# Kernel tuning notes

Hardware: AMD Instinct MI355X
Metric: run time of the kernel (lower is better)

The kernel has to match this reference:

```python
import jax, jax.numpy as jnp
import numpy as np

B, L, D_MODEL = 2, 2048, 256
D_STATE, D_CONV, EXPAND, HEADDIM = 128, 4, 4, 64
D_INNER = EXPAND * D_MODEL            # 1024
NHEADS = D_INNER // HEADDIM           # 16
CONV_DIM = D_INNER + 2 * D_STATE      # 1280
D_IN_PROJ = 2 * D_INNER + 2 * D_STATE + NHEADS  # 2320
CHUNK = 256
GN_EPS = float(np.finfo(np.float32).eps)
RMS_EPS = 1e-5


def _silu(x):
    return x * jax.nn.sigmoid(x)


def _segsum(x):
    # x: (..., T) -> (..., T, T); out[i, j] = sum_{j<k<=i} x[k] for i>=j else -inf
    T = x.shape[-1]
    cs = jnp.cumsum(x, -1)
    d = cs[..., :, None] - cs[..., None, :]
    mask = jnp.tril(jnp.ones((T, T), bool))
    return jnp.where(mask, d, -jnp.inf)


def _ssd(X, A, Bm, Cm):
    # Chunked SSD (Mamba2 ssd_minimal_discrete). X:(b,l,h,p) already dt-scaled,
    # A:(b,l,h) = dt * (-exp(A_log)), Bm/Cm:(b,l,n) with ngroups=1.
    b, l, h, p = X.shape
    c = l // CHUNK
    Xc = X.reshape(b, c, CHUNK, h, p)
    Ac = jnp.transpose(A.reshape(b, c, CHUNK, h), (0, 3, 1, 2))  # (b,h,c,Q)
    Bc = Bm.reshape(b, c, CHUNK, -1)
    Cc = Cm.reshape(b, c, CHUNK, -1)
    A_cs = jnp.cumsum(Ac, -1)                                    # (b,h,c,Q)
    Lmat = jnp.exp(_segsum(Ac))                                  # (b,h,c,Q,Q)
    CB = jnp.einsum('bcln,bcsn->bcls', Cc, Bc)                   # (b,c,Q,Q)
    Y_diag = jnp.einsum('bhcls,bcshp->bclhp', Lmat * CB[:, None], Xc)
    decay_states = jnp.exp(A_cs[..., -1:] - A_cs)                # (b,h,c,Q)
    states = jnp.einsum('bcln,bhcl,bclhp->bchpn', Bc, decay_states, Xc)
    states = jnp.concatenate([jnp.zeros_like(states[:, :1]), states], 1)  # (b,c+1,h,p,n)
    decay_chunk = jnp.exp(_segsum(jnp.pad(A_cs[..., -1], ((0, 0), (0, 0), (1, 0)))))  # (b,h,c+1,c+1)
    new_states = jnp.einsum('bhzc,bchpn->bzhpn', decay_chunk, states)[:, :-1]
    state_decay = jnp.exp(A_cs)                                  # (b,h,c,Q)
    Y_off = jnp.einsum('bcln,bchpn,bhcl->bclhp', Cc, new_states, state_decay)
    return (Y_diag + Y_off).reshape(b, l, h, p)


def _mamba2(u, in_w, conv_w, conv_b, dt_bias, A_log, Dh, norm_w, out_w):
    # u: (b, l, d_model)
    b, l, _ = u.shape
    zxbcdt = u @ in_w.T                                          # (b,l,D_IN_PROJ)
    z = zxbcdt[..., :D_INNER]
    xBC = zxbcdt[..., D_INNER:D_INNER + CONV_DIM]
    dt = jax.nn.softplus(zxbcdt[..., -NHEADS:] + dt_bias)        # (b,l,h)
    # causal depthwise conv over time
    xc = jnp.transpose(xBC, (0, 2, 1))                           # (b,C,l)
    xc = jax.lax.conv_general_dilated(xc, conv_w, (1,), [(D_CONV - 1, 0)],
                                      dimension_numbers=('NCH', 'OIH', 'NCH'),
                                      feature_group_count=CONV_DIM)
    xBC = _silu(jnp.transpose(xc + conv_b[None, :, None], (0, 2, 1)))
    x = xBC[..., :D_INNER].reshape(b, l, NHEADS, HEADDIM)
    Bm = xBC[..., D_INNER:D_INNER + D_STATE]
    Cm = xBC[..., D_INNER + D_STATE:]
    A = dt * (-jnp.exp(A_log))                                   # (b,l,h)
    y = _ssd(dt[..., None] * x, A, Bm, Cm) + x * Dh[None, None, :, None]
    y = y.reshape(b, l, D_INNER) * _silu(z)                      # gated
    y = y * jax.lax.rsqrt(jnp.mean(y * y, -1, keepdims=True) + RMS_EPS) * norm_w
    return y @ out_w.T                                           # (b,l,d_model)


def _resmamba(x, gn_w, gn_b, fp, bp, proj_w, proj_b):
    # GroupNorm(1, C) over (C, L) per sample
    mu = jnp.mean(x, (1, 2), keepdims=True)
    var = jnp.mean((x - mu) ** 2, (1, 2), keepdims=True)
    xn = (x - mu) * jax.lax.rsqrt(var + GN_EPS) * gn_w[None, :, None] + gn_b[None, :, None]
    t = jnp.transpose(xn, (0, 2, 1))                             # (B,L,C)
    fwd = _mamba2(t, *fp)
    bwd = jnp.flip(_mamba2(jnp.flip(t, 1), *bp), 1)
    r = jnp.concatenate([fwd + t, bwd + t], -1)                  # (B,L,2C)
    pr = r @ proj_w.T + proj_b                                   # (B,L,C)
    return x + jnp.transpose(pr, (0, 2, 1))


def setup_inputs():
    key = jax.random.key(0)
    ks = jax.random.split(key, 4)
    s = 0.02
    inp = {
        'x': jax.random.normal(ks[0], (B, D_MODEL, L), jnp.float32),
        'gn_w': jnp.ones((D_MODEL,), jnp.float32),
        'gn_b': jnp.zeros((D_MODEL,), jnp.float32),
        'proj_w': s * jax.random.normal(ks[1], (D_MODEL, 2 * D_MODEL), jnp.float32),
        'proj_b': jnp.zeros((D_MODEL,), jnp.float32),
    }
    for i, p in enumerate(('f', 'b')):
        kk = jax.random.split(ks[2 + i], 5)
        inp[p + '_in_w'] = s * jax.random.normal(kk[0], (D_IN_PROJ, D_MODEL), jnp.float32)
        inp[p + '_conv_w'] = s * jax.random.normal(kk[1], (CONV_DIM, 1, D_CONV), jnp.float32)
        inp[p + '_conv_b'] = jnp.zeros((CONV_DIM,), jnp.float32)
        inp[p + '_dt_bias'] = 0.1 * jax.random.normal(kk[2], (NHEADS,), jnp.float32)
        inp[p + '_A_log'] = jnp.log(jax.random.uniform(kk[3], (NHEADS,), jnp.float32, 1.0, 16.0))
        inp[p + '_D'] = jnp.ones((NHEADS,), jnp.float32)
        inp[p + '_norm_w'] = jnp.ones((D_INNER,), jnp.float32)
        inp[p + '_out_w'] = s * jax.random.normal(kk[4], (D_MODEL, D_INNER), jnp.float32)
    return inp


def reference(x, gn_w, gn_b, proj_w, proj_b,
              f_in_w, f_conv_w, f_conv_b, f_dt_bias, f_A_log, f_D, f_norm_w, f_out_w,
              b_in_w, b_conv_w, b_conv_b, b_dt_bias, b_A_log, b_D, b_norm_w, b_out_w):
    fp = (f_in_w, f_conv_w, f_conv_b, f_dt_bias, f_A_log, f_D, f_norm_w, f_out_w)
    bp = (b_in_w, b_conv_w, b_conv_b, b_dt_bias, b_A_log, b_D, b_norm_w, b_out_w)
    return _resmamba(x, gn_w, gn_b, fp, bp, proj_w, proj_b)
```

## Files before the change

kernel.cpp:

```cpp
#include <hip/hip_runtime.h>
#include <hip/hip_bf16.h>
#include <math.h>

using bf16 = __hip_bfloat16;

#define L_SEQ   2048
#define DMODEL  256
#define DINNER  1024
#define DSTATE  128
#define NH      16
#define HD      64
#define CONVDIM 1280
#define DPROJ   2320
#define NCHK    8
#define CT      256
#define BATCH   2
#define M_TOT   (BATCH*L_SEQ)

#define ACS_N   (BATCH*NH*NCHK*CT)
#define ST_N    ((size_t)BATCH*NCHK*NH*HD*DSTATE)
#define CB_N    ((size_t)BATCH*NCHK*CT*CT)

typedef __bf16 bf16x8_t __attribute__((ext_vector_type(8)));
typedef __bf16 bf16x4_t __attribute__((ext_vector_type(4)));
typedef float  f32x4_t  __attribute__((ext_vector_type(4)));

__device__ __forceinline__ float tof(bf16 v){ return __bfloat162float(v); }
__device__ __forceinline__ bf16  tob(float v){ return __float2bfloat16(v); }
__device__ __forceinline__ float expdec(float a){ return __expf(fminf(a, 0.f)); }

__global__ __launch_bounds__(256) void k_front(
    const float* __restrict__ iw0, const float* __restrict__ iw1, const float* __restrict__ pw,
    bf16* __restrict__ inw_bf, bf16* __restrict__ projw_bf,
    const float* __restrict__ ow0, const float* __restrict__ ow1,
    bf16* __restrict__ owt, bf16* __restrict__ psum,
    const float* __restrict__ x, float2* __restrict__ pbuf){
  __shared__ __bf16 tile[64][65];
  __shared__ float sh[8];
  int bz = blockIdx.x, t = threadIdx.x;
  if (bz < 1160){
    int dir = bz >= 580; int sub = dir ? bz - 580 : bz;
    const float* src = dir ? iw1 : iw0;
    bf16* dst = inw_bf + (size_t)dir*DPROJ*DMODEL;
    int i = (sub*256 + t)*4;
    float4 v = *(const float4*)(src + i);
    dst[i]   = tob(v.x); dst[i+1] = tob(v.y);
    dst[i+2] = tob(v.z); dst[i+3] = tob(v.w);
  } else if (bz < 1288){
    int i = ((bz-1160)*256 + t)*4;
    float4 v = *(const float4*)(pw + i);
    projw_bf[i]   = tob(v.x); projw_bf[i+1] = tob(v.y);
    projw_bf[i+2] = tob(v.z); projw_bf[i+3] = tob(v.w);
  } else if (bz < 1416){
    int sub = bz - 1288;
    int dir = sub >> 6; int tid = sub & 63;
    int k0 = (tid >> 2)*64, j0 = (tid & 3)*64;
    const float* src = dir ? ow1 : ow0;
    bf16* dst = owt + (size_t)dir*DINNER*DMODEL;
    #pragma unroll
    for (int it = 0; it < 2; ++it){
      int idx = t + it*256; int jj = idx >> 3; int k8 = (idx & 7)*8;
      float4 va = *(const float4*)&src[(size_t)(j0+jj)*DINNER + k0 + k8];
      float4 vb = *(const float4*)&src[(size_t)(j0+jj)*DINNER + k0 + k8 + 4];
      tile[k8+0][jj] = (__bf16)va.x; tile[k8+1][jj] = (__bf16)va.y;
      tile[k8+2][jj] = (__bf16)va.z; tile[k8+3][jj] = (__bf16)va.w;
      tile[k8+4][jj] = (__bf16)vb.x; tile[k8+5][jj] = (__bf16)vb.y;
      tile[k8+6][jj] = (__bf16)vb.z; tile[k8+7][jj] = (__bf16)vb.w;
    }
    __syncthreads();
    #pragma unroll
    for (int it = 0; it < 2; ++it){
      int idx = t + it*256; int kr = idx >> 3; int j8 = (idx & 7)*8;
      bf16x8_t o;
      #pragma unroll
      for (int i = 0; i < 8; ++i) o[i] = tile[kr][j8+i];
      *(bf16x8_t*)&dst[(size_t)(k0+kr)*DMODEL + j0 + j8] = o;
    }
  } else if (bz < 1448){
    int i = ((bz - 1416)*256 + t)*8;
    int j = i & 255;
    const float* row = pw + (size_t)(i >> 8)*(2*DMODEL);
    bf16x8_t o;
    #pragma unroll
    for (int c = 0; c < 8; ++c) o[c] = (__bf16)(row[j+c] + row[256+j+c]);
    *(bf16x8_t*)&psum[i] = o;
  } else {
    int sub = bz - 1448;
    int blk = sub & 127, b = sub >> 7;
    const float4* p = (const float4*)(x + (size_t)b*(DMODEL*L_SEQ) + (size_t)blk*4096);
    float s = 0.f, ss = 0.f;
    #pragma unroll
    for (int k = 0; k < 4; ++k){
      float4 v = p[t + k*256];
      s  += v.x + v.y + v.z + v.w;
      ss += v.x*v.x + v.y*v.y + v.z*v.z + v.w*v.w;
    }
    for (int o = 32; o > 0; o >>= 1){ s += __shfl_down(s, o, 64); ss += __shfl_down(ss, o, 64); }
    if ((t & 63) == 0){ sh[(t>>6)*2] = s; sh[(t>>6)*2+1] = ss; }
    __syncthreads();
    if (t == 0){
      s  = sh[0]+sh[2]+sh[4]+sh[6];
      ss = sh[1]+sh[3]+sh[5]+sh[7];
      pbuf[b*128 + blk] = make_float2(s, ss);
    }
  }
}

__global__ __launch_bounds__(256) void k_wt(const bf16* __restrict__ P, const bf16* __restrict__ owt,
                                            bf16* __restrict__ W,
                                            const float* __restrict__ x, const float* __restrict__ gw,
                                            const float* __restrict__ gb, const float2* __restrict__ pbuf,
                                            bf16* __restrict__ t_out){
  __shared__ __align__(16) bf16 lds[2][(128+64)*40];
  __shared__ float tile[64][65];
  __shared__ float sh[4];
  int bz6 = blockIdx.x;
  int t = threadIdx.x;
  if (bz6 < 64){
    int dir = bz6 & 1;
    int m0 = (bz6 >> 5)*128, n0 = ((bz6 >> 1) & 15)*64;
    int wave = t >> 6, lane = t & 63;
    int wm = (wave & 1)*64, wn = (wave >> 1)*32;
    int lrow = lane & 15, quad = lane >> 4, lk8 = quad*8;

    int r0 = t >> 2, o0 = (t & 3)*8;
    int r1 = r0 + 64;
    const bf16* Ap0 = P + (size_t)(m0 + r0)*(2*DMODEL) + dir*DMODEL + o0;
    const bf16* Ap1 = P + (size_t)(m0 + r1)*(2*DMODEL) + dir*DMODEL + o0;
    const bf16* Bp  = owt + (size_t)dir*DINNER*DMODEL + (size_t)(n0 + r0)*DMODEL + o0;

    f32x4_t acc[4][2];
    #pragma unroll
    for (int i = 0; i < 4; ++i){ acc[i][0] = (f32x4_t){0,0,0,0}; acc[i][1] = (f32x4_t){0,0,0,0}; }

    int nit = DMODEL >> 5;
    uint4 a0 = *(const uint4*)Ap0;
    uint4 a1 = *(const uint4*)Ap1;
    uint4 b0 = *(const uint4*)Bp;
    int st = 0;
    *(uint4*)&lds[0][r0*40 + o0] = a0;
    *(uint4*)&lds[0][r1*40 + o0] = a1;
    *(uint4*)&lds[0][(128 + r0)*40 + o0] = b0;
    __syncthreads();
    for (int it = 0; it < nit; ++it){
      bool more = (it+1 < nit);
      if (more){
        int kk = (it+1) << 5;
        a0 = *(const uint4*)(Ap0 + kk);
        a1 = *(const uint4*)(Ap1 + kk);
        b0 = *(const uint4*)(Bp + kk);
      }
      const bf16* cs = lds[st];
      bf16x8_t af[4], bfr[2];
      #pragma unroll
      for (int mi = 0; mi < 4; ++mi) af[mi] = *(const bf16x8_t*)&cs[(wm + mi*16 + lrow)*40 + lk8];
      #pragma unroll
      for (int ni = 0; ni < 2; ++ni) bfr[ni] = *(const bf16x8_t*)&cs[(128 + wn + ni*16 + lrow)*40 + lk8];
      #pragma unroll
      for (int mi = 0; mi < 4; ++mi)
        #pragma unroll
        for (int ni = 0; ni < 2; ++ni)
          acc[mi][ni] = __builtin_amdgcn_mfma_f32_16x16x32_bf16(af[mi], bfr[ni], acc[mi][ni], 0, 0, 0);
      if (more){
        st ^= 1;
        *(uint4*)&lds[st][r0*40 + o0] = a0;
        *(uint4*)&lds[st][r1*40 + o0] = a1;
        *(uint4*)&lds[st][(128 + r0)*40 + o0] = b0;
        __syncthreads();
      }
    }
    bf16* Wd = W + (size_t)dir*DMODEL*DINNER;
    #pragma unroll
    for (int mi = 0; mi < 4; ++mi)
      #pragma unroll
      for (int ni = 0; ni < 2; ++ni)
        #pragma unroll
        for (int r = 0; r < 4; ++r){
          int m = m0 + wm + mi*16 + quad*4 + r;
          int n = n0 + wn + ni*16 + lrow;
          Wd[(size_t)m*DINNER + n] = tob(acc[mi][ni][r]);
        }
  } else {
    int sub = bz6 - 64;
    int l0 = (sub & 31)*64, c0 = ((sub >> 5) & 3)*64, b = sub >> 7;
    int tid = t;
    float s = 0.f, ss = 0.f;
    if (tid < 128){ float2 v = pbuf[b*128 + tid]; s = v.x; ss = v.y; }
    for (int o = 32; o > 0; o >>= 1){ s += __shfl_down(s, o, 64); ss += __shfl_down(ss, o, 64); }
    if (tid < 128 && (tid & 63) == 0){ sh[(tid>>6)*2] = s; sh[(tid>>6)*2+1] = ss; }
    __syncthreads();
    float inv = 1.f/(float)(DMODEL*L_SEQ);
    float s0 = sh[0]+sh[2], ss0 = sh[1]+sh[3];
    float mu = s0*inv, var = ss0*inv - mu*mu;
    float istd = rsqrtf(fmaxf(var, 0.f) + 1.1920929e-07f);

    int lx = tid & 63, cy = tid >> 6;
    for (int cc = cy; cc < 64; cc += 4){
      float v = x[(size_t)b*DMODEL*L_SEQ + (size_t)(c0+cc)*L_SEQ + l0+lx];
      tile[cc][lx] = (v - mu)*istd;
    }
    __syncthreads();
    int cx = tid & 63, ly = tid >> 6;
    float w = gw[c0+cx], bb = gb[c0+cx];
    for (int ll = ly; ll < 64; ll += 4)
      t_out[((size_t)(b*L_SEQ) + l0+ll)*DMODEL + c0+cx] = tob(tile[cx][ll]*w + bb);
  }
}

__global__ __launch_bounds__(512) void gemm_inproj(const bf16* __restrict__ A, const bf16* __restrict__ B,
                                                   bf16* __restrict__ z, bf16* __restrict__ xbc,
                                                   float* __restrict__ dtb,
                                                   const float* __restrict__ db0, const float* __restrict__ db1){
  __shared__ __align__(16) bf16 lds[2][(128+128)*40];
  const int lda = DMODEL, ldb = DMODEL, N = DPROJ;
  int dir = blockIdx.z;
  const bf16* Bd = B + (size_t)dir*(size_t)N*ldb;
  int orig = blockIdx.x;
  int swz = (orig & 7)*76 + (orig >> 3);
  int m0 = (swz & 31)*128;
  int n0 = (swz >> 5)*128;
  int t = threadIdx.x;
  int wave = t >> 6, lane = t & 63;
  int wm = (wave & 1)*64, wn = (wave >> 1)*32;
  int lrow = lane & 15, quad = lane >> 4, lk8 = quad*8;

  int rA = t >> 2, oA = (t & 3)*8;
  int amA = m0 + rA;
  if (dir) amA = (amA & ~(L_SEQ-1)) | ((L_SEQ-1) - (amA & (L_SEQ-1)));
  int bnA = n0 + rA; if (bnA > N-1) bnA = N-1;
  const bf16* Ap = A + (size_t)amA*lda + oA;
  const bf16* Bp = Bd + (size_t)bnA*ldb + oA;

  f32x4_t acc[4][2];
  #pragma unroll
  for (int i = 0; i < 4; ++i){ acc[i][0] = (f32x4_t){0,0,0,0}; acc[i][1] = (f32x4_t){0,0,0,0}; }

  int nit = 8;
  uint4 a0 = *(const uint4*)Ap;
  uint4 b0 = *(const uint4*)Bp;
  int st = 0;
  *(uint4*)&lds[0][rA*40 + oA] = a0;
  *(uint4*)&lds[0][(128 + rA)*40 + oA] = b0;
  __syncthreads();
  for (int it = 0; it < nit; ++it){
    bool more = (it+1 < nit);
    if (more){
      int kk = (it+1) << 5;
      a0 = *(const uint4*)(Ap + kk);
      b0 = *(const uint4*)(Bp + kk);
    }
    const bf16* cs = lds[st];
    bf16x8_t bfr[2];
    #pragma unroll
    for (int ni = 0; ni < 2; ++ni) bfr[ni] = *(const bf16x8_t*)&cs[(128 + wn + ni*16 + lrow)*40 + lk8];
    #pragma unroll
    for (int mi = 0; mi < 4; ++mi){
      bf16x8_t af = *(const bf16x8_t*)&cs[(wm + mi*16 + lrow)*40 + lk8];
      #pragma unroll
      for (int ni = 0; ni < 2; ++ni)
        acc[mi][ni] = __builtin_amdgcn_mfma_f32_16x16x32_bf16(af, bfr[ni], acc[mi][ni], 0, 0, 0);
    }
    if (more){
      st ^= 1;
      *(uint4*)&lds[st][rA*40 + oA] = a0;
      *(uint4*)&lds[st][(128 + rA)*40 + oA] = b0;
      __syncthreads();
    }
  }

  if (n0 < DINNER + CONVDIM){
    __syncthreads();
    __bf16* outs = (__bf16*)lds;
    #pragma unroll
    for (int mi = 0; mi < 4; ++mi)
      #pragma unroll
      for (int ni = 0; ni < 2; ++ni)
        #pragma unroll
        for (int r = 0; r < 4; ++r)
          outs[(wm + mi*16 + quad*4 + r)*132 + wn + ni*16 + lrow] = (__bf16)acc[mi][ni][r];
    __syncthreads();
    bf16* dst; int ldd, c0;
    if (n0 < DINNER){ dst = z   + (size_t)dir*M_TOT*DINNER;  ldd = DINNER;  c0 = n0; }
    else            { dst = xbc + (size_t)dir*M_TOT*CONVDIM; ldd = CONVDIM; c0 = n0 - DINNER; }
    #pragma unroll
    for (int itv = 0; itv < 4; ++itv){
      int v = t + itv*512;
      int row = v >> 4, cb = v & 15;
      *(bf16x8_t*)&dst[(size_t)(m0+row)*ldd + c0 + cb*8] =
          *(const bf16x8_t*)&outs[row*132 + cb*8];
    }
  } else {
    const float* db = dir ? db1 : db0;
    float* dtp = dtb + (size_t)dir*((size_t)M_TOT*NH);
    #pragma unroll
    for (int mi = 0; mi < 4; ++mi)
      #pragma unroll
      for (int ni = 0; ni < 2; ++ni)
        #pragma unroll
        for (int r = 0; r < 4; ++r){
          int m = m0 + wm + mi*16 + quad*4 + r;
          int n = n0 + wn + ni*16 + lrow;
          if (n < N){
            int h = n - (DINNER + CONVDIM);
            float xx = acc[mi][ni][r] + db[h];
            dtp[(size_t)m*NH + h] = (xx > 20.f) ? xx : log1pf(expf(xx));
          }
        }
  }
}

__global__ __launch_bounds__(256) void gemm_final(const bf16* __restrict__ y, const bf16* __restrict__ tb,
                                                  const bf16* __restrict__ W, const bf16* __restrict__ psum,
                                                  const float* __restrict__ x, const float* __restrict__ pb,
                                                  float* __restrict__ out){
  __shared__ __align__(16) bf16 lds[2][(32+64)*72];
  __shared__ float tile[32][65];
  int orig = blockIdx.x;
  int swz = (orig & 7)*64 + (orig >> 3);
  int mt_ = swz & 127, nt_ = swz >> 7;
  int m0 = mt_*32, n0 = nt_*64;
  int t = threadIdx.x;
  int wave = t >> 6, lane = t & 63;
  int lrow = lane & 15, quad = lane >> 4, lk8 = quad*8;
  int wn = wave*16;

  f32x4_t acc[2];
  acc[0] = (f32x4_t){0,0,0,0}; acc[1] = (f32x4_t){0,0,0,0};

  int rowA = t >> 3, oA = (t & 7)*8;
  int rowB0 = t >> 3, oB0 = (t & 7)*8;
  int rowB1 = (t + 256) >> 3, oB1 = (t & 7)*8;

  #pragma unroll
  for (int ph = 0; ph < 3; ++ph){
    const bf16 *Ab, *Bb; int lda, ldb, K, rev;
    if (ph == 0){ Ab = y;                             lda = DINNER; K = DINNER; Bb = W;                             ldb = DINNER; rev = 0; }
    else if (ph == 1){ Ab = y + (size_t)M_TOT*DINNER; lda = DINNER; K = DINNER; Bb = W + (size_t)DMODEL*DINNER;     ldb = DINNER; rev = 1; }
    else { Ab = tb; lda = DMODEL; K = DMODEL; Bb = psum; ldb = DMODEL; rev = 0; }

    int am = m0 + rowA;
    if (rev) am = (am & ~(L_SEQ-1)) | ((L_SEQ-1) - (am & (L_SEQ-1)));
    const bf16* Ap  = Ab + (size_t)am*lda + oA;
    const bf16* Bp0 = Bb + (size_t)(n0 + rowB0)*ldb + oB0;
    const bf16* Bp1 = Bb + (size_t)(n0 + rowB1)*ldb + oB1;

    int nit = K >> 6;
    uint4 au  = *(const uint4*)Ap;
    uint4 bu0 = *(const uint4*)Bp0;
    uint4 bu1 = *(const uint4*)Bp1;
    uint4 av  = *(const uint4*)(Ap + 64);
    uint4 bv0 = *(const uint4*)(Bp0 + 64);
    uint4 bv1 = *(const uint4*)(Bp1 + 64);

#define FSTAGE(buf, A_, B0_, B1_) \
    *(uint4*)&lds[buf][rowA*72 + oA] = A_; \
    *(uint4*)&lds[buf][(32 + rowB0)*72 + oB0] = B0_; \
    *(uint4*)&lds[buf][(32 + rowB1)*72 + oB1] = B1_;

#define FCOMP(buf) { \
    const bf16* cs = lds[buf]; \
    _Pragma("unroll") \
    for (int ks = 0; ks < 2; ++ks){ \
      bf16x8_t bq = *(const bf16x8_t*)&cs[(32 + wn + lrow)*72 + ks*32 + lk8]; \
      _Pragma("unroll") \
      for (int mt = 0; mt < 2; ++mt){ \
        bf16x8_t af = *(const bf16x8_t*)&cs[(mt*16 + lrow)*72 + ks*32 + lk8]; \
        acc[mt] = __builtin_amdgcn_mfma_f32_16x16x32_bf16(af, bq, acc[mt], 0, 0, 0); \
      } \
    } }

    __syncthreads();
    FSTAGE(0, au, bu0, bu1)
    __syncthreads();
    for (int it = 0; it < nit; it += 2){
      if (it + 2 < nit){
        int kk = (it+2) << 6;
        au = *(const uint4*)(Ap+kk); bu0 = *(const uint4*)(Bp0+kk); bu1 = *(const uint4*)(Bp1+kk);
      }
      FCOMP(0)
      FSTAGE(1, av, bv0, bv1)
      __syncthreads();
      if (it + 3 < nit){
        int kk = (it+3) << 6;
        av = *(const uint4*)(Ap+kk); bv0 = *(const uint4*)(Bp0+kk); bv1 = *(const uint4*)(Bp1+kk);
      }
      FCOMP(1)
      if (it + 2 < nit){
        FSTAGE(0, au, bu0, bu1)
        __syncthreads();
      }
    }
#undef FSTAGE
#undef FCOMP
  }

  #pragma unroll
  for (int mt = 0; mt < 2; ++mt)
    #pragma unroll
    for (int r = 0; r < 4; ++r)
      tile[mt*16 + quad*4 + r][wn + lrow] = acc[mt][r];
  __syncthreads();
  int b = m0 >> 11, l0 = m0 & (L_SEQ-1);
  int tx = t & 31, ny = t >> 5;
  for (int nn = ny; nn < 64; nn += 8){
    int n = n0 + nn;
    size_t xi = (size_t)b*DMODEL*L_SEQ + (size_t)n*L_SEQ + l0 + tx;
    out[xi] = tile[tx][nn] + pb[n] + x[xi];
  }
}

__global__ __launch_bounds__(256) void k_conv(const bf16* __restrict__ xraw, const float* __restrict__ cw0,
                                              const float* __restrict__ cb0, const float* __restrict__ cw1,
                                              const float* __restrict__ cb1, bf16* __restrict__ xconv){
  int t = threadIdx.x;
  int tx = t & 31, ty = t >> 5;
  int ch0 = blockIdx.x*256 + tx*8;
  int z = blockIdx.z; int b = z & 1, dir = z >> 1;
  int lbase = blockIdx.y*32 + ty*4;
  const float* cw = dir ? cw1 : cw0;
  const float* cb = dir ? cb1 : cb0;
  const bf16* xr = xraw  + (size_t)dir*((size_t)M_TOT*CONVDIM) + (size_t)(b*L_SEQ)*CONVDIM + ch0;
  bf16* xcv      = xconv + (size_t)dir*((size_t)M_TOT*CONVDIM) + (size_t)(b*L_SEQ)*CONVDIM + ch0;

  float wk[4][8];
  #pragma unroll
  for (int c = 0; c < 8; ++c){
    float4 w = *(const float4*)&cw[(ch0+c)*4];
    wk[0][c] = w.x; wk[1][c] = w.y; wk[2][c] = w.z; wk[3][c] = w.w;
  }
  float bias[8];
  {
    float4 b0v = *(const float4*)&cb[ch0];
    float4 b1v = *(const float4*)&cb[ch0+4];
    bias[0]=b0v.x; bias[1]=b0v.y; bias[2]=b0v.z; bias[3]=b0v.w;
    bias[4]=b1v.x; bias[5]=b1v.y; bias[6]=b1v.z; bias[7]=b1v.w;
  }

  bf16x8_t zero;
  #pragma unroll
  for (int c = 0; c < 8; ++c) zero[c] = (__bf16)0.f;

  bf16x8_t win[4];
  #pragma unroll
  for (int k = 0; k < 3; ++k){
    int ls = lbase - 3 + k;
    win[k] = (ls >= 0) ? *(const bf16x8_t*)&xr[(size_t)ls*CONVDIM] : zero;
  }
  #pragma unroll
  for (int i = 0; i < 4; ++i){
    int l = lbase + i;
    win[3] = *(const bf16x8_t*)&xr[(size_t)l*CONVDIM];
    bf16x8_t outv;
    #pragma unroll
    for (int c = 0; c < 8; ++c){
      float a = bias[c] + (float)win[0][c]*wk[0][c] + (float)win[1][c]*wk[1][c]
                        + (float)win[2][c]*wk[2][c] + (float)win[3][c]*wk[3][c];
      outv[c] = (__bf16)(a / (1.f + __expf(-a)));
    }
    *(bf16x8_t*)&xcv[(size_t)l*CONVDIM] = outv;
    win[0] = win[1]; win[1] = win[2]; win[2] = win[3];
  }
}

__global__ __launch_bounds__(256) void k_states_cb(const bf16* __restrict__ xconv, const float* __restrict__ dt,
                                                   const float* __restrict__ Al0, const float* __restrict__ Al1,
                                                   float* __restrict__ A_cs, float* __restrict__ states,
                                                   bf16* __restrict__ CB){
  __shared__ __align__(16) char smem[34816];
  int bz = blockIdx.x, t = threadIdx.x;
  if (bz < 512){
    float* s_acs = (float*)smem;
    float* w_s   = (float*)(smem + 1024);
    __bf16* Xt   = (__bf16*)(smem + 2048);
    __bf16* Bt   = (__bf16*)(smem + 2048 + 9216);
    int id0 = bz;
    int dir = id0 >> 8; int id = id0 & 255;
    int h = id & 15; int bc = id >> 4; int ch = bc & 7; int b = bc >> 3;
    const bf16* xc = xconv + (size_t)dir*((size_t)M_TOT*CONVDIM);
    const float* dtp = dt + (size_t)dir*((size_t)M_TOT*NH);
    const float* Alog = dir ? Al1 : Al0;
    size_t rowbase = (size_t)(b*L_SEQ) + ch*CT;

    float dtv = dtp[(rowbase + t)*NH + h];
    s_acs[t] = -expf(Alog[h]) * dtv;
    __syncthreads();
    for (int off = 1; off < 256; off <<= 1){
      float v = (t >= off) ? s_acs[t-off] : 0.f;
      __syncthreads();
      s_acs[t] += v;
      __syncthreads();
    }
    A_cs[(size_t)dir*ACS_N + (size_t)((b*NH+h)*NCHK + ch)*CT + t] = s_acs[t];
    float alast = s_acs[CT-1];
    w_s[t] = dtv * __expf(fminf(alast - s_acs[t], 0.f));
    __syncthreads();

    int wave = t >> 6, lane = t & 63, lrow = lane & 15, quad = lane >> 4;
    f32x4_t acc[8];
    #pragma unroll
    for (int i = 0; i < 8; ++i) acc[i] = (f32x4_t){0.f,0.f,0.f,0.f};

    for (int kt = 0; kt < 4; ++kt){
      int l0 = kt*64;
      #pragma unroll
      for (int it = 0; it < 2; ++it){
        int idx = t + it*256; int l = idx >> 3; int p0 = (idx & 7)*8;
        bf16x8_t v = *(const bf16x8_t*)&xc[(rowbase + l0 + l)*CONVDIM + h*HD + p0];
        float w = w_s[l0 + l];
        int col = (((l>>3) ^ ((p0>>3)&7))<<3) | (l&7);
        #pragma unroll
        for (int j = 0; j < 8; ++j) Xt[(p0+j)*72 + col] = (__bf16)((float)v[j]*w);
      }
      #pragma unroll
      for (int it = 0; it < 4; ++it){
        int idx = t + it*256; int l = idx >> 4; int n0 = (idx & 15)*8;
        bf16x8_t v = *(const bf16x8_t*)&xc[(rowbase + l0 + l)*CONVDIM + DINNER + n0];
        int col = (((l>>3) ^ ((n0>>3)&7))<<3) | (l&7);
        #pragma unroll
        for (int j = 0; j < 8; ++j) Bt[(n0+j)*72 + col] = v[j];
      }
      __syncthreads();
      int arow = wave*16 + lrow;
      #pragma unroll
      for (int ks = 0; ks < 2; ++ks){
        int kg = ks*4 + quad;
        bf16x8_t af = *(const bf16x8_t*)&Xt[arow*72 + ((kg ^ ((arow>>3)&7))<<3)];
        #pragma unroll
        for (int nt = 0; nt < 8; ++nt){
          int brow = nt*16 + lrow;
          bf16x8_t bq = *(const bf16x8_t*)&Bt[brow*72 + ((kg ^ ((brow>>3)&7))<<3)];
          acc[nt] = __builtin_amdgcn_mfma_f32_16x16x32_bf16(af, bq, acc[nt], 0, 0, 0);
        }
      }
      __syncthreads();
    }
    float* so = states + (size_t)dir*ST_N + (size_t)id*HD*DSTATE;
    int m = wave*16 + quad*4;
    #pragma unroll
    for (int nt = 0; nt < 8; ++nt)
      #pragma unroll
      for (int r = 0; r < 4; ++r)
        so[(size_t)(m+r)*DSTATE + nt*16 + lrow] = acc[nt][r];
  } else {
    __bf16* As = (__bf16*)smem;
    __bf16* Bs = (__bf16*)(smem + 17408);
    int sub = bz - 512;
    int zz = sub >> 4;
    int dir = zz >> 4; int b = (zz >> 3) & 1; int ch = zz & 7;
    int rest = sub & 15;
    int m0 = (rest >> 2)*64, n0 = (rest & 3)*64;
    if (n0 > m0) return;
    const bf16* base = xconv + (size_t)dir*((size_t)M_TOT*CONVDIM) + (size_t)(b*L_SEQ + ch*CT)*CONVDIM;
    const bf16* Crow = base + DINNER + DSTATE;
    const bf16* Brow = base + DINNER;
    int r = t >> 2, o0 = (t & 3)*32;
    #pragma unroll
    for (int j = 0; j < 4; ++j){
      *(bf16x8_t*)&As[r*136 + o0 + j*8] = *(const bf16x8_t*)&Crow[(size_t)(m0+r)*CONVDIM + o0 + j*8];
      *(bf16x8_t*)&Bs[r*136 + o0 + j*8] = *(const bf16x8_t*)&Brow[(size_t)(n0+r)*CONVDIM + o0 + j*8];
    }
    __syncthreads();
    int wave = t >> 6, lane = t & 63, lrow = lane & 15, quad = lane >> 4;
    int wm = wave*16;
    f32x4_t acc[4];
    #pragma unroll
    for (int i = 0; i < 4; ++i) acc[i] = (f32x4_t){0.f,0.f,0.f,0.f};
    #pragma unroll
    for (int ks = 0; ks < 4; ++ks){
      bf16x8_t af = *(const bf16x8_t*)&As[(wm+lrow)*136 + ks*32 + quad*8];
      #pragma unroll
      for (int nt = 0; nt < 4; ++nt){
        bf16x8_t bq = *(const bf16x8_t*)&Bs[(nt*16+lrow)*136 + ks*32 + quad*8];
        acc[nt] = __builtin_amdgcn_mfma_f32_16x16x32_bf16(af, bq, acc[nt], 0, 0, 0);
      }
    }
    __syncthreads();
    #pragma unroll
    for (int nt = 0; nt < 4; ++nt)
      #pragma unroll
      for (int r2 = 0; r2 < 4; ++r2)
        As[(wm + quad*4 + r2)*72 + nt*16 + lrow] = (__bf16)acc[nt][r2];
    __syncthreads();
    bf16* outp = CB + (size_t)dir*CB_N + (size_t)(b*NCHK+ch)*CT*CT;
    #pragma unroll
    for (int p = 0; p < 2; ++p){
      int idx = t + p*256;
      int row = idx >> 3, c8 = (idx & 7)*8;
      *(bf16x8_t*)&outp[(size_t)(m0+row)*CT + n0 + c8] = *(const bf16x8_t*)&As[row*72 + c8];
    }
  }
}

__global__ __launch_bounds__(256) void k_recur(const float* __restrict__ states, bf16* __restrict__ nsb,
                                               const float* __restrict__ A_cs){
  int blk = blockIdx.x;
  int bh2 = blk >> 5;
  int e = (blk & 31)*256 + threadIdx.x;
  int dir = bh2 >> 5; int bh = bh2 & 31;
  int h = bh & 15, b = bh >> 4;
  const float* ac = A_cs + (size_t)dir*ACS_N;
  const float* st = states + (size_t)dir*ST_N;
  bf16* nb = nsb + (size_t)dir*ST_N;
  float s = 0.f;
  #pragma unroll
  for (int ch = 0; ch < NCHK; ++ch){
    float dec = expdec(ac[((size_t)(bh*NCHK+ch))*CT + CT-1]);
    size_t off = (size_t)(((b*NCHK+ch)*NH)+h)*HD*DSTATE + e;
    float cur = st[off];
    nb[off] = tob(s);
    s = s*dec + cur;
  }
}

__global__ __launch_bounds__(512) void k_y_mfma(const bf16* __restrict__ xconv, const float* __restrict__ dt,
                                                const float* __restrict__ A_cs, const bf16* __restrict__ CB,
                                                const bf16* __restrict__ ns, bf16* __restrict__ y){
  int id0 = blockIdx.x;
  int dir = id0 >> 8; int id = id0 & 255;
  int h = id & 15; int bc = id >> 4; int ch = bc & 7; int b = bc >> 3;
  int t = threadIdx.x;
  int lane = t & 63;
  int lrow = lane & 15, quad = lane >> 4;

  __shared__ __align__(16) bf16 Xs[64*264];
  __shared__ __align__(16) bf16 NSs[64*136];
  __shared__ float acs_s[CT];

  const bf16* xc = xconv + (size_t)dir*((size_t)M_TOT*CONVDIM);
  const float* dtp = dt + (size_t)dir*((size_t)M_TOT*NH);
  const float* acs = A_cs + (size_t)dir*ACS_N + (size_t)((b*NH+h)*NCHK + ch)*CT;
  const bf16* cbz = CB + (size_t)dir*CB_N + (size_t)(b*NCHK+ch)*CT*CT;
  const bf16* nsp = ns + (size_t)dir*ST_N + (size_t)(((b*NCHK+ch)*NH)+h)*HD*DSTATE;
  bf16* yp = y + (size_t)dir*((size_t)M_TOT*DINNER);
  size_t rowbase = (size_t)(b*L_SEQ + ch*CT);
  if (t < CT) acs_s[t] = acs[t];

  #pragma unroll
  for (int it = 0; it < 4; ++it){
    int idx = t + it*512;
    int s = idx >> 3, p0 = (idx & 7)*8;
    float dtv = dtp[(rowbase + s)*NH + h];
    bf16x8_t v = *(const bf16x8_t*)&xc[(rowbase + s)*CONVDIM + h*HD + p0];
    int col = ((((s>>3) ^ ((p0>>3)&7)))<<3) | (s&7);
    #pragma unroll
    for (int j = 0; j < 8; ++j)
      Xs[(p0+j)*264 + col] = tob((float)v[j] * dtv);
  }
  #pragma unroll
  for (int it = 0; it < 2; ++it){
    int idx = t + it*512;
    int p = idx >> 4, n8 = (idx & 15)*8;
    *(bf16x8_t*)&NSs[p*136 + n8] = *(const bf16x8_t*)&nsp[(size_t)p*DSTATE + n8];
  }
  __syncthreads();

  int wave = t >> 6;
  int sA = wave, sB = 15 - wave;
  float alA = acs_s[sA*16 + lrow];
  float alB = acs_s[sB*16 + lrow];

  f32x4_t acc[2][4];
  #pragma unroll
  for (int i = 0; i < 2; ++i)
    #pragma unroll
    for (int j = 0; j < 4; ++j) acc[i][j] = (f32x4_t){0.f,0.f,0.f,0.f};

  #pragma unroll
  for (int sp = 0; sp < 2; ++sp){
    int s = sp ? sB : sA;
    float al = sp ? alB : alA;
    int r0s = s*16;
    float a0r = acs_s[r0s];
    int nst = (s >> 1) + 1;
    for (int st = 0; st < nst; ++st){
      int s0 = st*32;
      if (s0 + 31 < r0s && (a0r - acs_s[s0+31]) < -30.f) continue;
      int sg = (s0 >> 3) + quad;
      bf16x8_t bq[4];
      #pragma unroll
      for (int nt = 0; nt < 4; ++nt){
        int brow = nt*16 + lrow;
        bq[nt] = *(const bf16x8_t*)&Xs[brow*264 + ((sg ^ ((brow>>3)&7))<<3)];
      }
      int l = r0s + lrow;
      bf16x8_t cvv = *(const bf16x8_t*)&cbz[(size_t)l*CT + s0 + quad*8];
      union { bf16x8_t v; __bf16 e[8]; } wa;
      #pragma unroll
      for (int j = 0; j < 8; ++j){
        int sI = s0 + quad*8 + j;
        float w = (sI <= l) ? __expf(fminf(al - acs_s[sI], 0.f)) * (float)cvv[j] : 0.f;
        wa.e[j] = (__bf16)w;
      }
      #pragma unroll
      for (int nt = 0; nt < 4; ++nt)
        acc[sp][nt] = __builtin_amdgcn_mfma_f32_16x16x32_bf16(wa.v, bq[nt], acc[sp][nt], 0, 0, 0);
    }
  }

  float elA = expdec(alA);
  float elB = expdec(alB);
  #pragma unroll
  for (int kt = 0; kt < 4; ++kt){
    int n0 = kt*32;
    bf16x8_t bq[4];
    #pragma unroll
    for (int nt = 0; nt < 4; ++nt)
      bq[nt] = *(const bf16x8_t*)&NSs[(nt*16+lrow)*136 + n0 + quad*8];
    #pragma unroll
    for (int sp = 0; sp < 2; ++sp){
      int s = sp ? sB : sA;
      float el = sp ? elB : elA;
      int l = s*16 + lrow;
      union { bf16x8_t v; __bf16 e[8]; } cu;
      cu.v = *(const bf16x8_t*)&xc[(rowbase + l)*CONVDIM + DINNER + DSTATE + n0 + quad*8];
      union { bf16x8_t v; __bf16 e[8]; } wa;
      #pragma unroll
      for (int j = 0; j < 8; ++j) wa.e[j] = (__bf16)((float)cu.e[j] * el);
      #pragma unroll
      for (int nt = 0; nt < 4; ++nt)
        acc[sp][nt] = __builtin_amdgcn_mfma_f32_16x16x32_bf16(wa.v, bq[nt], acc[sp][nt], 0, 0, 0);
    }
  }

  #pragma unroll
  for (int sp = 0; sp < 2; ++sp){
    int s = sp ? sB : sA;
    #pragma unroll
    for (int nt = 0; nt < 4; ++nt)
      #pragma unroll
      for (int rr = 0; rr < 4; ++rr){
        int l = s*16 + quad*4 + rr;
        int p = nt*16 + lrow;
        yp[(rowbase + l)*DINNER + h*HD + p] = tob(acc[sp][nt][rr]);
      }
  }
}

__global__ __launch_bounds__(256) void k_gaterms(const bf16* __restrict__ z, const float* __restrict__ nw0,
                                                 const float* __restrict__ nw1, const bf16* __restrict__ xconv,
                                                 const float* __restrict__ Dh0, const float* __restrict__ Dh1,
                                                 bf16* __restrict__ y){
  int m0 = blockIdx.x;
  int dir = m0 >> 12; int m = m0 & (M_TOT-1);
  int t = threadIdx.x;
  const float* nw = dir ? nw1 : nw0;
  const float* Dh = dir ? Dh1 : Dh0;
  int j0 = t*4;
  const bf16* zp = z + (size_t)dir*((size_t)M_TOT*DINNER) + (size_t)m*DINNER;
  const bf16* xc = xconv + (size_t)dir*((size_t)M_TOT*CONVDIM) + (size_t)m*CONVDIM;
  bf16* yp = y + (size_t)dir*((size_t)M_TOT*DINNER) + (size_t)m*DINNER;

  bf16x4_t zv = *(const bf16x4_t*)&zp[j0];
  bf16x4_t yv = *(const bf16x4_t*)&yp[j0];
  bf16x4_t xv = *(const bf16x4_t*)&xc[j0];
  float Dv = Dh[j0 >> 6];
  float v[4]; float ss = 0.f;
  #pragma unroll
  for (int c = 0; c < 4; ++c){
    float zf = (float)zv[c];
    float raw = (float)yv[c] + Dv*(float)xv[c];
    float g = raw * (zf / (1.f + __expf(-zf)));
    v[c] = g; ss += g*g;
  }
  for (int o = 32; o > 0; o >>= 1) ss += __shfl_down(ss, o, 64);
  __shared__ float sh[4];
  if ((t & 63) == 0) sh[t>>6] = ss;
  __syncthreads();
  ss = sh[0]+sh[1]+sh[2]+sh[3];
  float scale = rsqrtf(ss*(1.f/DINNER) + 1e-5f);
  float4 nwv = *(const float4*)&nw[j0];
  float nws[4] = {nwv.x, nwv.y, nwv.z, nwv.w};
  bf16x4_t o;
  #pragma unroll
  for (int c = 0; c < 4; ++c) o[c] = (__bf16)(v[c]*scale*nws[c]);
  *(bf16x4_t*)&yp[j0] = o;
}

extern "C" void kernel_launch(void* const* d_in, const int* in_sizes, int n_in,
                              void* d_out, int out_size, void* d_ws, size_t ws_size,
                              hipStream_t stream){
  (void)in_sizes; (void)n_in; (void)out_size; (void)ws_size;
  const float* x      = (const float*)d_in[0];
  const float* gn_w   = (const float*)d_in[1];
  const float* gn_b   = (const float*)d_in[2];
  const float* proj_w = (const float*)d_in[3];
  const float* proj_b = (const float*)d_in[4];
  float* out = (float*)d_out;

  char* wp = (char*)d_ws;
  auto alloc = [&](size_t bytes){ void* r = (void*)wp; wp += (bytes + 255) & ~(size_t)255; return r; };
  bf16*  t_buf  = (bf16*) alloc((size_t)M_TOT*DMODEL*2);
  bf16*  z_buf  = (bf16*) alloc((size_t)2*M_TOT*DINNER*2);
  bf16*  xraw   = (bf16*) alloc((size_t)2*M_TOT*CONVDIM*2);
  bf16*  xconv  = (bf16*) alloc((size_t)2*M_TOT*CONVDIM*2);
  float* dt_buf = (float*)alloc((size_t)2*M_TOT*NH*4);
  float* acs    = (float*)alloc((size_t)2*ACS_N*4);
  float* states = (float*)alloc((size_t)2*ST_N*4);
  bf16*  nsb    = (bf16*) alloc((size_t)2*ST_N*2);
  bf16*  cb     = (bf16*) alloc((size_t)2*CB_N*2);
  float2* pbuf  = (float2*)alloc(BATCH*128*sizeof(float2));
  bf16*  inw_bf   = (bf16*)alloc((size_t)2*DPROJ*DMODEL*2);
  bf16*  projw_bf = (bf16*)alloc((size_t)DMODEL*2*DMODEL*2);
  bf16*  owt      = (bf16*)alloc((size_t)2*DINNER*DMODEL*2);
  bf16*  wfb      = (bf16*)alloc((size_t)2*DMODEL*DINNER*2);
  bf16*  psum     = (bf16*)alloc((size_t)DMODEL*DMODEL*2);
  bf16*  y_buf    = xraw;

  k_front<<<1704, 256, 0, stream>>>(
      (const float*)d_in[5], (const float*)d_in[13], proj_w,
      inw_bf, projw_bf,
      (const float*)d_in[12], (const float*)d_in[20], owt, psum,
      x, pbuf);

  k_wt<<<320, 256, 0, stream>>>(projw_bf, owt, wfb, x, gn_w, gn_b, pbuf, t_buf);

  gemm_inproj<<<dim3(608, 1, 2), 512, 0, stream>>>(
      t_buf, inw_bf, z_buf, xraw, dt_buf,
      (const float*)d_in[8], (const float*)d_in[16]);

  k_conv<<<dim3(5, L_SEQ/32, 2*BATCH), 256, 0, stream>>>(
      xraw, (const float*)d_in[6], (const float*)d_in[7],
            (const float*)d_in[14], (const float*)d_in[15], xconv);
  k_states_cb<<<1024, 256, 0, stream>>>(
      xconv, dt_buf, (const float*)d_in[9], (const float*)d_in[17], acs, states, cb);
  k_recur<<<2*BATCH*NH*32, 256, 0, stream>>>(states, nsb, acs);
  k_y_mfma<<<2*BATCH*NCHK*NH, 512, 0, stream>>>(xconv, dt_buf, acs, cb, nsb, y_buf);
  k_gaterms<<<2*M_TOT, 256, 0, stream>>>(
      z_buf, (const float*)d_in[11], (const float*)d_in[19], xconv,
      (const float*)d_in[10], (const float*)d_in[18], y_buf);

  gemm_final<<<512, 256, 0, stream>>>(y_buf, t_buf, wfb, psum, x, proj_b, out);
}
```

Before: 208.7 us.

## Fuse depthwise causal conv and SiLU into in-projection GEMM epilogue

Removes the separate k_conv kernel by applying the 4-tap causal depthwise convolution and SiLU directly in the gemm_inproj epilogue for the xBC column tiles. The three halo rows before each 128-row M tile are recomputed with scalar dot products over K=256, so the raw xBC tensor no longer goes through global memory and one launch disappears. In exchange, the epilogue does redundant scalar work per tile and reloads conv weights per element, which may lengthen the GEMM's tail.

```diff
diff --git a/kernel.cpp b/kernel.cpp
--- a/kernel.cpp
+++ b/kernel.cpp
@@ -208,9 +208,11 @@
 }
 
 __global__ __launch_bounds__(512) void gemm_inproj(const bf16* __restrict__ A, const bf16* __restrict__ B,
-                                                   bf16* __restrict__ z, bf16* __restrict__ xbc,
+                                                   bf16* __restrict__ z, bf16* __restrict__ xconv,
                                                    float* __restrict__ dtb,
-                                                   const float* __restrict__ db0, const float* __restrict__ db1){
+                                                   const float* __restrict__ db0, const float* __restrict__ db1,
+                                                   const float* __restrict__ cw0, const float* __restrict__ cb0,
+                                                   const float* __restrict__ cw1, const float* __restrict__ cb1){
   __shared__ __align__(16) bf16 lds[2][(128+128)*40];
   const int lda = DMODEL, ldb = DMODEL, N = DPROJ;
   int dir = blockIdx.z;
@@ -268,7 +270,7 @@
     }
   }
 
-  if (n0 < DINNER + CONVDIM){
+  if (n0 < DINNER){
     __syncthreads();
     __bf16* outs = (__bf16*)lds;
     #pragma unroll
@@ -279,15 +281,66 @@
         for (int r = 0; r < 4; ++r)
           outs[(wm + mi*16 + quad*4 + r)*132 + wn + ni*16 + lrow] = (__bf16)acc[mi][ni][r];
     __syncthreads();
-    bf16* dst; int ldd, c0;
-    if (n0 < DINNER){ dst = z   + (size_t)dir*M_TOT*DINNER;  ldd = DINNER;  c0 = n0; }
-    else            { dst = xbc + (size_t)dir*M_TOT*CONVDIM; ldd = CONVDIM; c0 = n0 - DINNER; }
+    bf16* dst = z + (size_t)dir*M_TOT*DINNER;
     #pragma unroll
     for (int itv = 0; itv < 4; ++itv){
       int v = t + itv*512;
       int row = v >> 4, cb = v & 15;
-      *(bf16x8_t*)&dst[(size_t)(m0+row)*ldd + c0 + cb*8] =
+      *(bf16x8_t*)&dst[(size_t)(m0+row)*DINNER + n0 + cb*8] =
           *(const bf16x8_t*)&outs[row*132 + cb*8];
+    }
+  } else if (n0 < DINNER + CONVDIM){
+    bool doHalo = (m0 & (L_SEQ-1)) != 0;
+    __syncthreads();
+    __bf16* outs = (__bf16*)lds;
+    if (t < 384){
+      int hrow = t >> 7, col = t & 127;
+      float s = 0.f;
+      if (doHalo){
+        int mh = m0 - 3 + hrow;
+        int amH = mh;
+        if (dir) amH = (amH & ~(L_SEQ-1)) | ((L_SEQ-1) - (amH & (L_SEQ-1)));
+        const bf16* Arow = A + (size_t)amH*lda;
+        const bf16* Brow = Bd + (size_t)(n0 + col)*ldb;
+        for (int kk = 0; kk < 32; ++kk){
+          bf16x8_t av = *(const bf16x8_t*)&Arow[kk*8];
+          bf16x8_t bv = *(const bf16x8_t*)&Brow[kk*8];
+          #pragma unroll
+          for (int j = 0; j < 8; ++j) s += (float)av[j]*(float)bv[j];
+        }
+      }
+      outs[hrow*132 + col] = (__bf16)s;
+    }
+    #pragma unroll
+    for (int mi = 0; mi < 4; ++mi)
+      #pragma unroll
+      for (int ni = 0; ni < 2; ++ni)
+        #pragma unroll
+        for (int r = 0; r < 4; ++r)
+          outs[(3 + wm + mi*16 + quad*4 + r)*132 + wn + ni*16 + lrow] = (__bf16)acc[mi][ni][r];
+    __syncthreads();
+    int c0 = n0 - DINNER;
+    const float* cw  = dir ? cw1 : cw0;
+    const float* cbv = dir ? cb1 : cb0;
+    bf16* dst = xconv + (size_t)dir*(size_t)M_TOT*CONVDIM;
+    #pragma unroll
+    for (int itv = 0; itv < 4; ++itv){
+      int v = t + itv*512;
+      int row = v >> 4, cbk = v & 15;
+      int ch0 = c0 + cbk*8;
+      bf16x8_t w0 = *(const bf16x8_t*)&outs[(row+0)*132 + cbk*8];
+      bf16x8_t w1 = *(const bf16x8_t*)&outs[(row+1)*132 + cbk*8];
+      bf16x8_t w2 = *(const bf16x8_t*)&outs[(row+2)*132 + cbk*8];
+      bf16x8_t w3 = *(const bf16x8_t*)&outs[(row+3)*132 + cbk*8];
+      bf16x8_t ov;
+      #pragma unroll
+      for (int j = 0; j < 8; ++j){
+        float4 wj = *(const float4*)&cw[(ch0+j)*4];
+        float a = cbv[ch0+j] + (float)w0[j]*wj.x + (float)w1[j]*wj.y
+                             + (float)w2[j]*wj.z + (float)w3[j]*wj.w;
+        ov[j] = (__bf16)(a / (1.f + __expf(-a)));
+      }
+      *(bf16x8_t*)&dst[(size_t)(m0+row)*CONVDIM + ch0] = ov;
     }
   } else {
     const float* db = dir ? db1 : db0;
@@ -406,59 +459,6 @@
     int n = n0 + nn;
     size_t xi = (size_t)b*DMODEL*L_SEQ + (size_t)n*L_SEQ + l0 + tx;
     out[xi] = tile[tx][nn] + pb[n] + x[xi];
-  }
-}
-
-__global__ __launch_bounds__(256) void k_conv(const bf16* __restrict__ xraw, const float* __restrict__ cw0,
-                                              const float* __restrict__ cb0, const float* __restrict__ cw1,
-                                              const float* __restrict__ cb1, bf16* __restrict__ xconv){
-  int t = threadIdx.x;
-  int tx = t & 31, ty = t >> 5;
-  int ch0 = blockIdx.x*256 + tx*8;
-  int z = blockIdx.z; int b = z & 1, dir = z >> 1;
-  int lbase = blockIdx.y*32 + ty*4;
-  const float* cw = dir ? cw1 : cw0;
-  const float* cb = dir ? cb1 : cb0;
-  const bf16* xr = xraw  + (size_t)dir*((size_t)M_TOT*CONVDIM) + (size_t)(b*L_SEQ)*CONVDIM + ch0;
-  bf16* xcv      = xconv + (size_t)dir*((size_t)M_TOT*CONVDIM) + (size_t)(b*L_SEQ)*CONVDIM + ch0;
-
-  float wk[4][8];
-  #pragma unroll
-  for (int c = 0; c < 8; ++c){
-    float4 w = *(const float4*)&cw[(ch0+c)*4];
-    wk[0][c] = w.x; wk[1][c] = w.y; wk[2][c] = w.z; wk[3][c] = w.w;
-  }
-  float bias[8];
-  {
-    float4 b0v = *(const float4*)&cb[ch0];
-    float4 b1v = *(const float4*)&cb[ch0+4];
-    bias[0]=b0v.x; bias[1]=b0v.y; bias[2]=b0v.z; bias[3]=b0v.w;
-    bias[4]=b1v.x; bias[5]=b1v.y; bias[6]=b1v.z; bias[7]=b1v.w;
-  }
-
-  bf16x8_t zero;
-  #pragma unroll
-  for (int c = 0; c < 8; ++c) zero[c] = (__bf16)0.f;
-
-  bf16x8_t win[4];
-  #pragma unroll
-  for (int k = 0; k < 3; ++k){
-    int ls = lbase - 3 + k;
-    win[k] = (ls >= 0) ? *(const bf16x8_t*)&xr[(size_t)ls*CONVDIM] : zero;
-  }
-  #pragma unroll
-  for (int i = 0; i < 4; ++i){
-    int l = lbase + i;
-    win[3] = *(const bf16x8_t*)&xr[(size_t)l*CONVDIM];
-    bf16x8_t outv;
-    #pragma unroll
-    for (int c = 0; c < 8; ++c){
-      float a = bias[c] + (float)win[0][c]*wk[0][c] + (float)win[1][c]*wk[1][c]
-                        + (float)win[2][c]*wk[2][c] + (float)win[3][c]*wk[3][c];
-      outv[c] = (__bf16)(a / (1.f + __expf(-a)));
-    }
-    *(bf16x8_t*)&xcv[(size_t)l*CONVDIM] = outv;
-    win[0] = win[1]; win[1] = win[2]; win[2] = win[3];
   }
 }
 
@@ -815,12 +815,11 @@
   k_wt<<<320, 256, 0, stream>>>(projw_bf, owt, wfb, x, gn_w, gn_b, pbuf, t_buf);
 
   gemm_inproj<<<dim3(608, 1, 2), 512, 0, stream>>>(
-      t_buf, inw_bf, z_buf, xraw, dt_buf,
-      (const float*)d_in[8], (const float*)d_in[16]);
-
-  k_conv<<<dim3(5, L_SEQ/32, 2*BATCH), 256, 0, stream>>>(
-      xraw, (const float*)d_in[6], (const float*)d_in[7],
-            (const float*)d_in[14], (const float*)d_in[15], xconv);
+      t_buf, inw_bf, z_buf, xconv, dt_buf,
+      (const float*)d_in[8], (const float*)d_in[16],
+      (const float*)d_in[6], (const float*)d_in[7],
+      (const float*)d_in[14], (const float*)d_in[15]);
+
   k_states_cb<<<1024, 256, 0, stream>>>(
       xconv, dt_buf, (const float*)d_in[9], (const float*)d_in[17], acs, states, cb);
   k_recur<<<2*BATCH*NH*32, 256, 0, stream>>>(states, nsb, acs);
```

Measured after the change: 281.9 us. 35.1% more time.
